# Kernel tuning notes

Measured on AMD Instinct MI355X. Metric: run time of the kernel, lower is better.

The kernel has to match this reference:

```python
import jax, jax.numpy as jnp
import numpy as np

B, N, E = 2, 2048, 1024   # batch, seq_len, embed_dim (= hidden_dim)
H, HD = 16, 64            # num_heads, head_dim


def setup_inputs() -> dict:
    key = jax.random.key(0)
    ks = jax.random.split(key, 6)
    w = lambda k: jax.random.normal(k, (E, E), jnp.float32) * 0.02
    return {
        "x": jax.random.normal(ks[0], (B, N, E), jnp.float32),
        "Wq": w(ks[1]), "bq": jnp.zeros((E,), jnp.float32),
        "Wk": w(ks[2]), "bk": jnp.zeros((E,), jnp.float32),
        "Wv": w(ks[3]), "bv": jnp.zeros((E,), jnp.float32),
        "Wu": w(ks[4]), "bu": jnp.zeros((E,), jnp.float32),
        "Wo": w(ks[5]), "bo": jnp.zeros((E,), jnp.float32),
        "ln_g": jnp.ones((E,), jnp.float32),
        "ln_b": jnp.zeros((E,), jnp.float32),
    }


def reference(x, Wq, bq, Wk, bk, Wv, bv, Wu, bu, Wo, bo, ln_g, ln_b):
    # projections (torch Linear: x @ W.T + b)
    q = x @ Wq.T + bq
    k = x @ Wk.T + bk
    v = jax.nn.silu(x @ Wv.T + bv)   # uv_act = swish
    u = jax.nn.silu(x @ Wu.T + bu)
    # split heads: [B, N, H*HD] -> [B, H, N, HD]
    split = lambda t: t.reshape(B, N, H, HD).transpose(0, 2, 1, 3)
    q, k, v = split(q), split(k), split(v)
    # non-softmax attention: ReLU on scaled energy (no causal mask)
    energy = jnp.einsum("bhnd,bhmd->bhnm", q, k) / jnp.float32(np.sqrt(HD))
    energy = jax.nn.relu(energy)
    out = jnp.einsum("bhnm,bhmd->bhnd", energy, v)
    # merge heads: [B, H, N, HD] -> [B, N, H*HD]
    out = out.transpose(0, 2, 1, 3).reshape(B, N, H * HD)
    # layernorm over hidden_dim
    mu = out.mean(-1, keepdims=True)
    var = out.var(-1, keepdims=True)
    out = (out - mu) * jax.lax.rsqrt(var + 1e-5) * ln_g + ln_b
    # gate and output projection
    out = u * out
    return out @ Wo.T + bo
```

## Files before the change

### kernel.cpp

```cpp
#include <hip/hip_runtime.h>
#include <stdint.h>

typedef unsigned short u16;
typedef __attribute__((ext_vector_type(8))) short short8;
typedef __attribute__((ext_vector_type(4))) short short4v;
typedef __attribute__((ext_vector_type(4))) float floatx4;
typedef __attribute__((ext_vector_type(4))) int intx4;

#define B_ 2
#define N_ 2048
#define E_ 1024
#define H_ 16
#define HD_ 64
#define M_TOT (B_ * N_)

__device__ __forceinline__ float bf2f(u16 h) {
    union { unsigned u; float f; } c; c.u = ((unsigned)h) << 16; return c.f;
}
__device__ __forceinline__ u16 f2bf(float f) {
    union { float f; unsigned u; } c; c.f = f;
    unsigned r = c.u + 0x7FFFu + ((c.u >> 16) & 1u);
    return (u16)(r >> 16);
}
__device__ __forceinline__ float silu_f(float x) { return x / (1.f + __expf(-x)); }

template <typename T> __device__ __forceinline__ void store_out(T* p, float v);
template <> __device__ __forceinline__ void store_out<u16>(u16* p, float v)    { *p = f2bf(v); }
template <> __device__ __forceinline__ void store_out<float>(float* p, float v) { *p = v; }

__device__ __forceinline__ void gll16(const void* g, void* l) {
    __builtin_amdgcn_global_load_lds(
        (const __attribute__((address_space(1))) void*)g,
        (__attribute__((address_space(3))) void*)l,
        16, 0, 0);
}

#if __has_builtin(__builtin_amdgcn_mfma_f32_16x16x16bf16_1k)
__device__ __forceinline__ floatx4 mfma16(short4v a, short4v b, floatx4 c) {
    return __builtin_amdgcn_mfma_f32_16x16x16bf16_1k(a, b, c, 0, 0, 0);
}
#else
__device__ __forceinline__ floatx4 mfma16(short4v a, short4v b, floatx4 c) {
    floatx4 d;
    asm volatile("v_mfma_f32_16x16x16_bf16 %0, %1, %2, %3\n\ts_nop 3"
                 : "=v"(d) : "v"(a), "v"(b), "v"(c));
    return d;
}
#endif

__device__ __forceinline__ short4v relu_pack(floatx4 s) {
    union { float f; unsigned u; } c0, c1, c2, c3;
    c0.f = fmaxf(s[0], 0.f); c1.f = fmaxf(s[1], 0.f);
    c2.f = fmaxf(s[2], 0.f); c3.f = fmaxf(s[3], 0.f);
    unsigned lo = __builtin_amdgcn_perm(c1.u + 0x8000u, c0.u + 0x8000u, 0x07060302);
    unsigned hi = __builtin_amdgcn_perm(c3.u + 0x8000u, c2.u + 0x8000u, 0x07060302);
    union { unsigned v[2]; short4v s4; } r; r.v[0] = lo; r.v[1] = hi;
    return r.s4;
}

__launch_bounds__(256, 4)
__global__ void cvt6(const float* __restrict__ s0, const float* __restrict__ s1,
                     const float* __restrict__ s2, const float* __restrict__ s3,
                     const float* __restrict__ s4, const float* __restrict__ s5,
                     u16* __restrict__ d0, u16* __restrict__ d1,
                     u16* __restrict__ d2, u16* __restrict__ d3,
                     u16* __restrict__ d4, u16* __restrict__ d5)
{
    const int z = blockIdx.z;
    if (z > 0 && blockIdx.x >= E_ * E_ / 2048) return;
    const float* src = (z == 0) ? s0 : (z == 1) ? s1 : (z == 2) ? s2
                     : (z == 3) ? s3 : (z == 4) ? s4 : s5;
    u16* dst         = (z == 0) ? d0 : (z == 1) ? d1 : (z == 2) ? d2
                     : (z == 3) ? d3 : (z == 4) ? d4 : d5;
    const int i = (blockIdx.x * 256 + threadIdx.x) * 8;
    floatx4 a = *(const floatx4*)(src + i);
    floatx4 b = *(const floatx4*)(src + i + 4);
    union { u16 h[8]; intx4 v; } o;
    o.h[0] = f2bf(a[0]); o.h[1] = f2bf(a[1]); o.h[2] = f2bf(a[2]); o.h[3] = f2bf(a[3]);
    o.h[4] = f2bf(b[0]); o.h[5] = f2bf(b[1]); o.h[6] = f2bf(b[2]); o.h[7] = f2bf(b[3]);
    *(intx4*)(dst + i) = o.v;
}

template <typename OutT>
__launch_bounds__(256, 2)
__global__ void gemm4(const u16* __restrict__ A,
                      const u16* __restrict__ W0, const u16* __restrict__ W1,
                      const u16* __restrict__ W2, const u16* __restrict__ W3,
                      const float* __restrict__ bi0, const float* __restrict__ bi1,
                      const float* __restrict__ bi2, const float* __restrict__ bi3,
                      OutT* __restrict__ O0, OutT* __restrict__ O1,
                      OutT* __restrict__ O2, OutT* __restrict__ O3,
                      int actmask, int scalemask, int K)
{
    __shared__ u16 a_lds[128 * 32];
    __shared__ u16 b_lds[128 * 32];

    const int z = blockIdx.z;
    const u16* W    = (z == 0) ? W0 : (z == 1) ? W1 : (z == 2) ? W2 : W3;
    const float* Bi = (z == 0) ? bi0 : (z == 1) ? bi1 : (z == 2) ? bi2 : bi3;
    OutT* Out       = (z == 0) ? O0 : (z == 1) ? O1 : (z == 2) ? O2 : O3;
    const bool act = (actmask >> z) & 1;
    const float osc = ((scalemask >> z) & 1) ? 0.125f : 1.0f;

    const int t    = threadIdx.x;
    const int wave = t >> 6, lane = t & 63, quad = lane >> 4, l16 = lane & 15;
    const int wm = wave >> 1, wn = wave & 1;
    const int m0 = blockIdx.y * 128;
    const int n0 = blockIdx.x * 128;

    floatx4 acc[4][4];
    const floatx4 fz = {0.f, 0.f, 0.f, 0.f};
    for (int i = 0; i < 4; i++)
        for (int j = 0; j < 4; j++) acc[i][j] = fz;

    const int ar = t >> 2;
    const int ac = (t & 3) * 8;
    const u16* Ag0 = A + (size_t)(m0 + ar) * K + ac;
    const u16* Ag1 = A + (size_t)(m0 + 64 + ar) * K + ac;
    const u16* Bg0 = W + (size_t)(n0 + ar) * K + ac;
    const u16* Bg1 = W + (size_t)(n0 + 64 + ar) * K + ac;
    u16* al0 = a_lds + wave * 512;
    u16* al1 = a_lds + 2048 + wave * 512;
    u16* bl0 = b_lds + wave * 512;
    u16* bl1 = b_lds + 2048 + wave * 512;

    for (int k0 = 0; k0 < K; k0 += 32) {
        __syncthreads();
        gll16(Ag0 + k0, al0);
        gll16(Ag1 + k0, al1);
        gll16(Bg0 + k0, bl0);
        gll16(Bg1 + k0, bl1);
        __syncthreads();

        short8 af[4], bfr[4];
        for (int i = 0; i < 4; i++)
            af[i]  = *(const short8*)&a_lds[(wm * 64 + i * 16 + l16) * 32 + quad * 8];
        for (int j = 0; j < 4; j++)
            bfr[j] = *(const short8*)&b_lds[(wn * 64 + j * 16 + l16) * 32 + quad * 8];
        for (int i = 0; i < 4; i++)
            for (int j = 0; j < 4; j++)
                acc[i][j] = __builtin_amdgcn_mfma_f32_16x16x32_bf16(af[i], bfr[j], acc[i][j], 0, 0, 0);
    }

    float bias_v[4];
    for (int j = 0; j < 4; j++) bias_v[j] = Bi[n0 + wn * 64 + j * 16 + l16];

    for (int i = 0; i < 4; i++) {
        const int row = m0 + wm * 64 + i * 16 + quad * 4;
        for (int j = 0; j < 4; j++) {
            const int col = n0 + wn * 64 + j * 16 + l16;
            for (int r = 0; r < 4; r++) {
                float v = acc[i][j][r] + bias_v[j];
                if (act) v = silu_f(v);
                v *= osc;
                store_out<OutT>(&Out[(size_t)(row + r) * E_ + col], v);
            }
        }
    }
}

__launch_bounds__(256, 4)
__global__ void vtrans(const u16* __restrict__ V, u16* __restrict__ VT)
{
    __shared__ u16 ts[64 * 72];
    const int bh = blockIdx.y;
    const int b = bh >> 4, h = bh & 15;
    const int n0 = blockIdx.x * 64;
    const int t = threadIdx.x;
    const int r = t >> 2, seg = (t & 3) * 16;

    const u16* src = V + ((size_t)b * N_ + n0 + r) * E_ + h * HD_ + seg;
    intx4 x0 = *(const intx4*)(src);
    intx4 x1 = *(const intx4*)(src + 8);
    *(intx4*)&ts[r * 72 + seg]     = x0;
    *(intx4*)&ts[r * 72 + seg + 8] = x1;
    __syncthreads();

    union { u16 h[16]; intx4 v[2]; } buf;
    for (int j = 0; j < 16; j++) buf.h[j] = ts[(seg + j) * 72 + r];
    u16* dst = VT + ((size_t)bh * HD_ + r) * N_ + n0 + seg;
    *(intx4*)(dst)     = buf.v[0];
    *(intx4*)(dst + 8) = buf.v[1];
}

#define LQ 72
#define KSPLIT 4
#define KCHUNK (N_ / KSPLIT)

__launch_bounds__(256, 4)
__global__ void attn(const u16* __restrict__ Q, const u16* __restrict__ Kk,
                     const u16* __restrict__ VT,
                     u16* __restrict__ P0, u16* __restrict__ P1,
                     u16* __restrict__ P2, u16* __restrict__ P3)
{
    __shared__ u16 k_lds[64 * LQ];
    __shared__ u16 vt_lds[64 * LQ];

    const int bh = blockIdx.y;
    const int b = bh >> 4, h = bh & 15;
    const int z = blockIdx.z;
    u16* __restrict__ Oa = (z == 0) ? P0 : (z == 1) ? P1 : (z == 2) ? P2 : P3;
    const int key_base = z * KCHUNK;

    const int t = threadIdx.x;
    const int wave = t >> 6, lane = t & 63, quad = lane >> 4, l16 = lane & 15;
    const int q0 = blockIdx.x * 128 + wave * 32;
    const size_t base = (size_t)b * N_ * E_ + h * HD_;

    short8 aq[2][2];
    for (int mi = 0; mi < 2; mi++)
        for (int ks = 0; ks < 2; ks++)
            aq[mi][ks] = *(const short8*)(Q + base + (size_t)(q0 + mi * 16 + l16) * E_ + ks * 32 + quad * 8);

    floatx4 o[2][4];
    const floatx4 fz = {0.f, 0.f, 0.f, 0.f};
    for (int mi = 0; mi < 2; mi++)
        for (int nd = 0; nd < 4; nd++) o[mi][nd] = fz;

    const int srow = t >> 2;
    const int sseg = (t & 3) * 16;
    const u16* Ksrc = Kk + base + (size_t)(key_base + srow) * E_ + sseg;
    const u16* Vsrc = VT + ((size_t)bh * HD_ + srow) * N_ + key_base + sseg;

    for (int kt = 0; kt < KCHUNK / 64; kt++) {
        __syncthreads();
        intx4 k0v = *(const intx4*)(Ksrc + (size_t)(kt * 64) * E_);
        intx4 k1v = *(const intx4*)(Ksrc + (size_t)(kt * 64) * E_ + 8);
        intx4 v0v = *(const intx4*)(Vsrc + kt * 64);
        intx4 v1v = *(const intx4*)(Vsrc + kt * 64 + 8);
        *(intx4*)&k_lds[srow * LQ + sseg]      = k0v;
        *(intx4*)&k_lds[srow * LQ + sseg + 8]  = k1v;
        *(intx4*)&vt_lds[srow * LQ + sseg]     = v0v;
        *(intx4*)&vt_lds[srow * LQ + sseg + 8] = v1v;
        __syncthreads();

        for (int n = 0; n < 4; n++) {
            short8 ka0 = *(const short8*)&k_lds[(n * 16 + l16) * LQ + quad * 8];
            short8 ka1 = *(const short8*)&k_lds[(n * 16 + l16) * LQ + 32 + quad * 8];
            short4v bv[4];
            for (int nd = 0; nd < 4; nd++)
                bv[nd] = *(const short4v*)&vt_lds[(nd * 16 + l16) * LQ + n * 16 + quad * 4];

            for (int mi = 0; mi < 2; mi++) {
                floatx4 st = __builtin_amdgcn_mfma_f32_16x16x32_bf16(ka0, aq[mi][0], fz, 0, 0, 0);
                st = __builtin_amdgcn_mfma_f32_16x16x32_bf16(ka1, aq[mi][1], st, 0, 0, 0);
                short4v sa = relu_pack(st);
                for (int nd = 0; nd < 4; nd++)
                    o[mi][nd] = mfma16(sa, bv[nd], o[mi][nd]);
            }
        }
    }

    for (int mi = 0; mi < 2; mi++)
        for (int nd = 0; nd < 4; nd++)
            for (int r = 0; r < 4; r++)
                Oa[(size_t)(b * N_ + q0 + mi * 16 + quad * 4 + r) * E_ + h * HD_ + nd * 16 + l16] =
                    f2bf(o[mi][nd][r]);
}

__launch_bounds__(256, 4)
__global__ void ln_gate(const u16* __restrict__ P0, const u16* __restrict__ P1,
                        const u16* __restrict__ P2, const u16* __restrict__ P3,
                        const u16* __restrict__ U,
                        const float* __restrict__ G, const float* __restrict__ Bb,
                        u16* __restrict__ Out)
{
    const int row = blockIdx.x;
    const int t = threadIdx.x;
    const size_t idx = (size_t)row * E_ + t * 4;
    const short4v a0 = *(const short4v*)(P0 + idx);
    const short4v a1 = *(const short4v*)(P1 + idx);
    const short4v a2 = *(const short4v*)(P2 + idx);
    const short4v a3 = *(const short4v*)(P3 + idx);
    floatx4 v;
    for (int i = 0; i < 4; i++)
        v[i] = bf2f((u16)a0[i]) + bf2f((u16)a1[i]) + bf2f((u16)a2[i]) + bf2f((u16)a3[i]);
    float s  = v[0] + v[1] + v[2] + v[3];
    float ss = v[0] * v[0] + v[1] * v[1] + v[2] * v[2] + v[3] * v[3];
    for (int off = 32; off; off >>= 1) {
        s  += __shfl_down(s, off, 64);
        ss += __shfl_down(ss, off, 64);
    }
    __shared__ float red[8];
    const int wave = t >> 6, lane = t & 63;
    if (lane == 0) { red[wave] = s; red[4 + wave] = ss; }
    __syncthreads();
    const float S  = red[0] + red[1] + red[2] + red[3];
    const float SS = red[4] + red[5] + red[6] + red[7];
    const float mu  = S * (1.f / E_);
    const float var = SS * (1.f / E_) - mu * mu;
    const float rstd = rsqrtf(var + 1e-5f);

    short4v outv;
    for (int i = 0; i < 4; i++) {
        const int e = t * 4 + i;
        float y = (v[i] - mu) * rstd * G[e] + Bb[e];
        y *= bf2f(U[idx + i]);
        outv[i] = (short)f2bf(y);
    }
    *(short4v*)(Out + idx) = outv;
}

extern "C" void kernel_launch(void* const* d_in, const int* in_sizes, int n_in,
                              void* d_out, int out_size, void* d_ws, size_t ws_size,
                              hipStream_t stream)
{
    const float* x   = (const float*)d_in[0];
    const float* Wq  = (const float*)d_in[1];
    const float* bq  = (const float*)d_in[2];
    const float* Wk  = (const float*)d_in[3];
    const float* bk  = (const float*)d_in[4];
    const float* Wv  = (const float*)d_in[5];
    const float* bv  = (const float*)d_in[6];
    const float* Wu  = (const float*)d_in[7];
    const float* bu  = (const float*)d_in[8];
    const float* Wo  = (const float*)d_in[9];
    const float* bo  = (const float*)d_in[10];
    const float* lng = (const float*)d_in[11];
    const float* lnb = (const float*)d_in[12];

    char* ws = (char*)d_ws;
    u16*  qw  = (u16*)(ws);
    u16*  kw  = (u16*)(ws + 8388608);
    u16*  vw  = (u16*)(ws + 16777216);
    u16*  uw  = (u16*)(ws + 25165824);
    u16*  p0  = (u16*)(ws + 33554432);
    u16*  p1  = (u16*)(ws + 41943040);
    u16*  xb  = (u16*)(ws + 50331648);
    u16*  vt  = (u16*)(ws + 50331648);
    u16*  wbq = (u16*)(ws + 58720256);
    u16*  wbk = (u16*)(ws + 60817408);
    u16*  wbv = (u16*)(ws + 62914560);
    u16*  wbu = (u16*)(ws + 65011712);
    u16*  wbo = (u16*)(ws + 67108864);
    u16*  gw  = (u16*)(ws);

    float* out = (float*)d_out;
    u16*  p2  = (u16*)d_out;
    u16*  p3  = (u16*)d_out + 4194304;

    const dim3 blk(256, 1, 1);

    cvt6<<<dim3(M_TOT * E_ / 2048, 1, 6), blk, 0, stream>>>(
        x, Wq, Wk, Wv, Wu, Wo, xb, wbq, wbk, wbv, wbu, wbo);
    gemm4<u16><<<dim3(8, 32, 4), blk, 0, stream>>>(xb, wbq, wbk, wbv, wbu,
                                                   bq, bk, bv, bu,
                                                   qw, kw, vw, uw, 0xC, 0x1, E_);
    vtrans<<<dim3(N_ / 64, B_ * H_, 1), blk, 0, stream>>>(vw, vt);
    attn<<<dim3(N_ / 128, B_ * H_, KSPLIT), blk, 0, stream>>>(qw, kw, vt, p0, p1, p2, p3);
    ln_gate<<<dim3(M_TOT, 1, 1), blk, 0, stream>>>(p0, p1, p2, p3, uw, lng, lnb, gw);
    gemm4<float><<<dim3(8, 32, 1), blk, 0, stream>>>(gw, wbo, wbo, wbo, wbo,
                                                     bo, bo, bo, bo,
                                                     out, out, out, out, 0x0, 0x0, E_);
}
```

Before: 238.1 us.

## Enlarge attention query tile, use 16x16x32 MFMA for PV and async V loads

```diff
diff --git a/kernel.cpp b/kernel.cpp
--- a/kernel.cpp
+++ b/kernel.cpp
@@ -34,19 +34,6 @@
         (__attribute__((address_space(3))) void*)l,
         16, 0, 0);
 }
-
-#if __has_builtin(__builtin_amdgcn_mfma_f32_16x16x16bf16_1k)
-__device__ __forceinline__ floatx4 mfma16(short4v a, short4v b, floatx4 c) {
-    return __builtin_amdgcn_mfma_f32_16x16x16bf16_1k(a, b, c, 0, 0, 0);
-}
-#else
-__device__ __forceinline__ floatx4 mfma16(short4v a, short4v b, floatx4 c) {
-    floatx4 d;
-    asm volatile("v_mfma_f32_16x16x16_bf16 %0, %1, %2, %3\n\ts_nop 3"
-                 : "=v"(d) : "v"(a), "v"(b), "v"(c));
-    return d;
-}
-#endif
 
 __device__ __forceinline__ short4v relu_pack(floatx4 s) {
     union { float f; unsigned u; } c0, c1, c2, c3;
@@ -183,18 +170,18 @@
     *(intx4*)(dst + 8) = buf.v[1];
 }
 
-#define LQ 72
+#define LK 72
 #define KSPLIT 4
 #define KCHUNK (N_ / KSPLIT)
 
-__launch_bounds__(256, 4)
+__launch_bounds__(256, 2)
 __global__ void attn(const u16* __restrict__ Q, const u16* __restrict__ Kk,
                      const u16* __restrict__ VT,
                      u16* __restrict__ P0, u16* __restrict__ P1,
                      u16* __restrict__ P2, u16* __restrict__ P3)
 {
-    __shared__ u16 k_lds[64 * LQ];
-    __shared__ u16 vt_lds[64 * LQ];
+    __shared__ u16 k_lds[64 * LK];
+    __shared__ u16 v_lds[64 * 64];
 
     const int bh = blockIdx.y;
     const int b = bh >> 4, h = bh & 15;
@@ -204,54 +191,67 @@
 
     const int t = threadIdx.x;
     const int wave = t >> 6, lane = t & 63, quad = lane >> 4, l16 = lane & 15;
-    const int q0 = blockIdx.x * 128 + wave * 32;
+    const int q0 = blockIdx.x * 256 + wave * 64;
     const size_t base = (size_t)b * N_ * E_ + h * HD_;
 
-    short8 aq[2][2];
-    for (int mi = 0; mi < 2; mi++)
+    short8 aq[4][2];
+    for (int mi = 0; mi < 4; mi++)
         for (int ks = 0; ks < 2; ks++)
             aq[mi][ks] = *(const short8*)(Q + base + (size_t)(q0 + mi * 16 + l16) * E_ + ks * 32 + quad * 8);
 
-    floatx4 o[2][4];
+    floatx4 o[4][4];
     const floatx4 fz = {0.f, 0.f, 0.f, 0.f};
-    for (int mi = 0; mi < 2; mi++)
+    for (int mi = 0; mi < 4; mi++)
         for (int nd = 0; nd < 4; nd++) o[mi][nd] = fz;
 
-    const int srow = t >> 2;
-    const int sseg = (t & 3) * 16;
+    const int srow = t >> 2, sseg = (t & 3) * 16;
+    const int prow = (srow & 32) + (((srow >> 2) & 1) << 4)
+                   + (((srow >> 3) & 3) << 2) + (srow & 3);
     const u16* Ksrc = Kk + base + (size_t)(key_base + srow) * E_ + sseg;
-    const u16* Vsrc = VT + ((size_t)bh * HD_ + srow) * N_ + key_base + sseg;
+    u16* kdst = &k_lds[prow * LK + sseg];
+
+    const int vd0 = wave * 8 + (lane >> 3);
+    const int vk0 = (lane & 7) * 8;
+    const u16* Vsrc0 = VT + ((size_t)bh * HD_ + vd0) * N_ + key_base + vk0;
+    const u16* Vsrc1 = VT + ((size_t)bh * HD_ + vd0 + 32) * N_ + key_base + vk0;
+    u16* vdst0 = v_lds + wave * 512;
+    u16* vdst1 = v_lds + 2048 + wave * 512;
 
     for (int kt = 0; kt < KCHUNK / 64; kt++) {
         __syncthreads();
-        intx4 k0v = *(const intx4*)(Ksrc + (size_t)(kt * 64) * E_);
-        intx4 k1v = *(const intx4*)(Ksrc + (size_t)(kt * 64) * E_ + 8);
-        intx4 v0v = *(const intx4*)(Vsrc + kt * 64);
-        intx4 v1v = *(const intx4*)(Vsrc + kt * 64 + 8);
-        *(intx4*)&k_lds[srow * LQ + sseg]      = k0v;
-        *(intx4*)&k_lds[srow * LQ + sseg + 8]  = k1v;
-        *(intx4*)&vt_lds[srow * LQ + sseg]     = v0v;
-        *(intx4*)&vt_lds[srow * LQ + sseg + 8] = v1v;
+        const size_t kof = (size_t)(kt * 64) * E_;
+        gll16(Vsrc0 + kt * 64, vdst0);
+        gll16(Vsrc1 + kt * 64, vdst1);
+        intx4 k0v = *(const intx4*)(Ksrc + kof);
+        intx4 k1v = *(const intx4*)(Ksrc + kof + 8);
+        *(intx4*)(kdst)     = k0v;
+        *(intx4*)(kdst + 8) = k1v;
         __syncthreads();
 
-        for (int n = 0; n < 4; n++) {
-            short8 ka0 = *(const short8*)&k_lds[(n * 16 + l16) * LQ + quad * 8];
-            short8 ka1 = *(const short8*)&k_lds[(n * 16 + l16) * LQ + 32 + quad * 8];
-            short4v bv[4];
+        for (int g = 0; g < 2; g++) {
+            short8 ka[2][2];
+            for (int tp = 0; tp < 2; tp++)
+                for (int ks = 0; ks < 2; ks++)
+                    ka[tp][ks] = *(const short8*)&k_lds[(g * 32 + tp * 16 + l16) * LK + ks * 32 + quad * 8];
+            short8 bv[4];
             for (int nd = 0; nd < 4; nd++)
-                bv[nd] = *(const short4v*)&vt_lds[(nd * 16 + l16) * LQ + n * 16 + quad * 4];
-
-            for (int mi = 0; mi < 2; mi++) {
-                floatx4 st = __builtin_amdgcn_mfma_f32_16x16x32_bf16(ka0, aq[mi][0], fz, 0, 0, 0);
-                st = __builtin_amdgcn_mfma_f32_16x16x32_bf16(ka1, aq[mi][1], st, 0, 0, 0);
-                short4v sa = relu_pack(st);
+                bv[nd] = *(const short8*)&v_lds[(nd * 16 + l16) * 64 + g * 32 + quad * 8];
+
+            for (int mi = 0; mi < 4; mi++) {
+                floatx4 c0 = __builtin_amdgcn_mfma_f32_16x16x32_bf16(ka[0][0], aq[mi][0], fz, 0, 0, 0);
+                c0 = __builtin_amdgcn_mfma_f32_16x16x32_bf16(ka[0][1], aq[mi][1], c0, 0, 0, 0);
+                floatx4 c1 = __builtin_amdgcn_mfma_f32_16x16x32_bf16(ka[1][0], aq[mi][0], fz, 0, 0, 0);
+                c1 = __builtin_amdgcn_mfma_f32_16x16x32_bf16(ka[1][1], aq[mi][1], c1, 0, 0, 0);
+                union { short4v h[2]; short8 s8; } sf;
+                sf.h[0] = relu_pack(c0);
+                sf.h[1] = relu_pack(c1);
                 for (int nd = 0; nd < 4; nd++)
-                    o[mi][nd] = mfma16(sa, bv[nd], o[mi][nd]);
+                    o[mi][nd] = __builtin_amdgcn_mfma_f32_16x16x32_bf16(sf.s8, bv[nd], o[mi][nd], 0, 0, 0);
             }
         }
     }
 
-    for (int mi = 0; mi < 2; mi++)
+    for (int mi = 0; mi < 4; mi++)
         for (int nd = 0; nd < 4; nd++)
             for (int r = 0; r < 4; r++)
                 Oa[(size_t)(b * N_ + q0 + mi * 16 + quad * 4 + r) * E_ + h * HD_ + nd * 16 + l16] =
@@ -347,7 +347,7 @@
                                                    bq, bk, bv, bu,
                                                    qw, kw, vw, uw, 0xC, 0x1, E_);
     vtrans<<<dim3(N_ / 64, B_ * H_, 1), blk, 0, stream>>>(vw, vt);
-    attn<<<dim3(N_ / 128, B_ * H_, KSPLIT), blk, 0, stream>>>(qw, kw, vt, p0, p1, p2, p3);
+    attn<<<dim3(N_ / 256, B_ * H_, KSPLIT), blk, 0, stream>>>(qw, kw, vt, p0, p1, p2, p3);
     ln_gate<<<dim3(M_TOT, 1, 1), blk, 0, stream>>>(p0, p1, p2, p3, uw, lng, lnb, gw);
     gemm4<float><<<dim3(8, 32, 1), blk, 0, stream>>>(gw, wbo, wbo, wbo, wbo,
                                                      bo, bo, bo, bo,
```

New measurement: 228.2 us. 4.2% less time.
